# Kernel optimization log

Measured on AMD Instinct MI355X. Metric: run time of the kernel, lower is better.

Reference implementation:

```python
import jax, jax.numpy as jnp
import numpy as np

BETA = 0.25


def _nearest(flat, cb):
    # flat: [N, D], cb: [K, D]
    dist = (jnp.sum(flat * flat, axis=1, keepdims=True)
            + jnp.sum(cb * cb, axis=1)
            - 2.0 * flat @ cb.T)  # [N, K]
    inds = jnp.argmin(dist, axis=1)  # [N]
    q = cb[inds]                     # gather == one_hot @ cb
    return q, inds


def _mse(a, b):
    d = a - b
    return jnp.mean(d * d)


def _closeness(latents, q_det, q_noisy=None):
    adj = q_det if q_noisy is None else q_noisy
    return (BETA * _mse(latents, jax.lax.stop_gradient(q_det))
            + _mse(adj, jax.lax.stop_gradient(latents)))


def setup_inputs() -> dict:
    key = jax.random.key(0)
    k1, k2, k3 = jax.random.split(key, 3)
    B, S, C, K, D = 8192, 64, 16, 8192, 1024
    x = jax.random.normal(k1, (B, S, C), dtype=jnp.float32)
    # codebooks initialized uniform(-1/K, 1/K) and mean-centered, as in initial_codebook
    inv = 1.0 / K
    in_cb = jax.random.uniform(k2, (K, D), dtype=jnp.float32, minval=-inv, maxval=inv)
    in_cb = in_cb - jnp.mean(in_cb, axis=0)
    out_cb = jax.random.uniform(k3, (K, D), dtype=jnp.float32, minval=-inv, maxval=inv)
    out_cb = out_cb - jnp.mean(out_cb, axis=0)
    return {"x": x, "in_codebook": in_cb, "out_codebook": out_cb}


def reference(x, in_codebook, out_codebook):
    B, S, C = x.shape
    flat = x.reshape(B, S * C)  # 'b s c -> b (s c)'
    # in-codebook quantization (noisy=False)
    x_q, x_inds = _nearest(flat, in_codebook)
    # reconstruct(encoding_inds): codebook gather (abstract in base class)
    recon = in_codebook[x_inds]
    # out-codebook quantization; noise_std = 0.0 so noisy inds == det inds
    rq_det, r_inds = _nearest(recon, out_codebook)
    rq_noisy = rq_det
    # straight-through output
    out = flat + jax.lax.stop_gradient(rq_noisy - flat)
    loss = (_closeness(flat, rq_det, rq_noisy)
            + _closeness(flat, x_q)
            + _closeness(recon, rq_det, rq_noisy))
    return out.reshape(B, S, C), loss
```

## Files before the change

### kernel.cpp

```cpp
#include <hip/hip_runtime.h>
#include <hip/hip_bf16.h>
#include <stdint.h>

#define N_ROWS 8192
#define DDIM   1024
#define KCB    8192

#define SX   (6.0f / 127.0f)
#define SCB  (1.3e-4f / 127.0f)
#define NS1  (1.0f / (SX  * SCB))
#define NS2  (1.0f / (SCB * SCB))

typedef int   int32x4 __attribute__((ext_vector_type(4)));

__device__ __forceinline__ int quant_pack4(float4 v, float inv) {
  int q0 = (int)rintf(fminf(fmaxf(v.x * inv, -127.f), 127.f));
  int q1 = (int)rintf(fminf(fmaxf(v.y * inv, -127.f), 127.f));
  int q2 = (int)rintf(fminf(fmaxf(v.z * inv, -127.f), 127.f));
  int q3 = (int)rintf(fminf(fmaxf(v.w * inv, -127.f), 127.f));
  return (q0 & 255) | ((q1 & 255) << 8) | ((q2 & 255) << 16) | (q3 << 24);
}

__global__ __launch_bounds__(256) void prep_all(const float* __restrict__ x,
                                                const float* __restrict__ incb,
                                                const float* __restrict__ outcb,
                                                int* __restrict__ x8,
                                                int* __restrict__ incb8,
                                                int* __restrict__ outcb8,
                                                float* __restrict__ norms_in,
                                                float* __restrict__ norms_out) {
  int b = blockIdx.x;
  int t = threadIdx.x;
  if (b >= 2 * KCB) {
    int i = (b - 2 * KCB) * 256 + t;
    float4 v = ((const float4*)x)[i];
    x8[i] = quant_pack4(v, 1.0f / SX);
    return;
  }
  const float* cb = (b < KCB) ? incb : outcb;
  int*  cb8       = (b < KCB) ? incb8 : outcb8;
  float* norms    = (b < KCB) ? norms_in : norms_out;
  float  nscale   = (b < KCB) ? NS1 : NS2;
  int r = (b < KCB) ? b : b - KCB;
  float4 v = ((const float4*)(cb + (size_t)r * DDIM))[t];
  cb8[(size_t)r * 256 + t] = quant_pack4(v, 1.0f / SCB);
  float s = v.x*v.x + v.y*v.y + v.z*v.z + v.w*v.w;
  #pragma unroll
  for (int sh = 32; sh > 0; sh >>= 1) s += __shfl_down(s, sh, 64);
  __shared__ float wsum[4];
  int lane = t & 63, w = t >> 6;
  if (lane == 0) wsum[w] = s;
  __syncthreads();
  if (t == 0) norms[r] = (wsum[0] + wsum[1] + wsum[2] + wsum[3]) * nscale;
}

#define BM 256
#define BN 128
#define BKB 64
#define NT  (DDIM / BKB)

#define AS1 __attribute__((address_space(1)))
#define AS3 __attribute__((address_space(3)))

#define BAR() do { asm volatile("" ::: "memory"); __builtin_amdgcn_s_barrier(); \
                   asm volatile("" ::: "memory"); } while (0)

__global__ __launch_bounds__(512) void gemm_argmin(
    const char* __restrict__ A0, const char* __restrict__ B0,
    const float* __restrict__ n0, unsigned long long* __restrict__ pk0,
    const char* __restrict__ A1, const char* __restrict__ B1,
    const float* __restrict__ n1, unsigned long long* __restrict__ pk1)
{
  __shared__ char As[3][BM * BKB];
  __shared__ char Bs[3][BN * BKB];

  const char* __restrict__ A     = blockIdx.z ? A1 : A0;
  const char* __restrict__ B     = blockIdx.z ? B1 : B0;
  const float* __restrict__ norms = blockIdx.z ? n1 : n0;
  unsigned long long* __restrict__ packed = blockIdx.z ? pk1 : pk0;

  const int t    = threadIdx.x;
  const int lane = t & 63;
  const int wid  = t >> 6;
  const int wr   = wid >> 1, wc = wid & 1;
  const int la   = lane & 15, lg = lane >> 4;
  const int brow = blockIdx.x * BM;
  const int bcol = blockIdx.y * BN;

  const int srow = t >> 2;
  const int scol = (((t & 3) ^ ((srow >> 1) & 3)) << 4);

  #define STAGE(tt, dA, dB) do {                                              \
    const char* ga0 = A + (size_t)(brow + srow)       * DDIM + (tt) * BKB + scol; \
    const char* ga1 = A + (size_t)(brow + 128 + srow) * DDIM + (tt) * BKB + scol; \
    const char* gb  = B + (size_t)(bcol + srow)       * DDIM + (tt) * BKB + scol; \
    __builtin_amdgcn_global_load_lds((AS1 void*)ga0, (AS3 void*)((dA) + t * 16),          16, 0, 0); \
    __builtin_amdgcn_global_load_lds((AS1 void*)ga1, (AS3 void*)((dA) + (512 + t) * 16),  16, 0, 0); \
    __builtin_amdgcn_global_load_lds((AS1 void*)gb,  (AS3 void*)((dB) + t * 16),          16, 0, 0); \
  } while (0)

  int aoff[4], boff[4];
  #pragma unroll
  for (int mi = 0; mi < 4; ++mi) {
    int r = wr * 64 + mi * 16 + la;
    aoff[mi] = r * BKB + ((lg ^ ((r >> 1) & 3)) << 4);
  }
  #pragma unroll
  for (int ni = 0; ni < 4; ++ni) {
    int r = wc * 64 + ni * 16 + la;
    boff[ni] = r * BKB + ((lg ^ ((r >> 1) & 3)) << 4);
  }

  int32x4 acc[4][4];
  #pragma unroll
  for (int i = 0; i < 4; ++i)
    #pragma unroll
    for (int j = 0; j < 4; ++j) acc[i][j] = (int32x4){0, 0, 0, 0};

  STAGE(0, As[0], Bs[0]);
  STAGE(1, As[1], Bs[1]);
  asm volatile("s_waitcnt vmcnt(3)" ::: "memory");
  BAR();

  for (int kt = 0; kt < NT; ++kt) {
    int nx = kt + 2;
    if (nx < NT) {
      int bi = nx % 3;
      STAGE(nx, As[bi], Bs[bi]);
    }
    const char* curA = As[kt % 3];
    const char* curB = Bs[kt % 3];
    int32x4 af[4], bfr[4];
    #pragma unroll
    for (int mi = 0; mi < 4; ++mi) af[mi]  = *(const int32x4*)(curA + aoff[mi]);
    #pragma unroll
    for (int ni = 0; ni < 4; ++ni) bfr[ni] = *(const int32x4*)(curB + boff[ni]);
    #pragma unroll
    for (int mi = 0; mi < 4; ++mi)
      #pragma unroll
      for (int ni = 0; ni < 4; ++ni)
        acc[mi][ni] = __builtin_amdgcn_mfma_i32_16x16x64_i8(af[mi], bfr[ni], acc[mi][ni], 0, 0, 0);
    if (kt < NT - 2)       { asm volatile("s_waitcnt vmcnt(3)" ::: "memory"); BAR(); }
    else if (kt == NT - 2) { asm volatile("s_waitcnt vmcnt(0)" ::: "memory"); BAR(); }
  }
  #undef STAGE

  float nrm[4]; int colg[4];
  #pragma unroll
  for (int ni = 0; ni < 4; ++ni) {
    colg[ni] = bcol + wc * 64 + ni * 16 + la;
    nrm[ni]  = norms[colg[ni]];
  }
  #pragma unroll
  for (int mi = 0; mi < 4; ++mi) {
    #pragma unroll
    for (int j = 0; j < 4; ++j) {
      float best = nrm[0] - 2.0f * (float)acc[mi][0][j];
      int  bidx  = colg[0];
      #pragma unroll
      for (int ni = 1; ni < 4; ++ni) {
        float v = nrm[ni] - 2.0f * (float)acc[mi][ni][j];
        if (v < best || (v == best && colg[ni] < bidx)) { best = v; bidx = colg[ni]; }
      }
      #pragma unroll
      for (int s = 1; s < 16; s <<= 1) {
        float ov = __shfl_xor(best, s, 64);
        int   oi = __shfl_xor(bidx, s, 64);
        if (ov < best || (ov == best && oi < bidx)) { best = ov; bidx = oi; }
      }
      if (la == 0) {
        int row = brow + wr * 64 + mi * 16 + lg * 4 + j;
        unsigned int ub = __float_as_uint(best);
        ub = (ub & 0x80000000u) ? ~ub : (ub | 0x80000000u);
        unsigned long long pk = ((unsigned long long)ub << 32) | (unsigned int)bidx;
        atomicMin(packed + row, pk);
      }
    }
  }
}

__global__ __launch_bounds__(256) void finalize_k(const float* __restrict__ x,
                                                  const float* __restrict__ incb,
                                                  const float* __restrict__ outcb,
                                                  const unsigned long long* __restrict__ p1,
                                                  const unsigned long long* __restrict__ p2,
                                                  float* __restrict__ out,
                                                  double* __restrict__ accum) {
  int n  = blockIdx.x;
  int xi = (int)(p1[n] & 0xffffffffull);
  int ri = (int)(p2[xi] & 0xffffffffull);
  int t  = threadIdx.x;
  float4 f = ((const float4*)(x     + (size_t)n  * DDIM))[t];
  float4 a = ((const float4*)(incb  + (size_t)xi * DDIM))[t];
  float4 r = ((const float4*)(outcb + (size_t)ri * DDIM))[t];
  ((float4*)(out + (size_t)n * DDIM))[t] = r;
  float s = 0.f;
  { float d1 = f.x - r.x, d2 = f.x - a.x, d3 = a.x - r.x; s += d1*d1 + d2*d2 + d3*d3; }
  { float d1 = f.y - r.y, d2 = f.y - a.y, d3 = a.y - r.y; s += d1*d1 + d2*d2 + d3*d3; }
  { float d1 = f.z - r.z, d2 = f.z - a.z, d3 = a.z - r.z; s += d1*d1 + d2*d2 + d3*d3; }
  { float d1 = f.w - r.w, d2 = f.w - a.w, d3 = a.w - r.w; s += d1*d1 + d2*d2 + d3*d3; }
  #pragma unroll
  for (int sh = 32; sh > 0; sh >>= 1) s += __shfl_down(s, sh, 64);
  __shared__ float wsum[4];
  int lane = t & 63, w = t >> 6;
  if (lane == 0) wsum[w] = s;
  __syncthreads();
  if (t == 0) atomicAdd(accum, (double)(wsum[0] + wsum[1] + wsum[2] + wsum[3]));
}

__global__ void write_loss(const double* __restrict__ accum, float* __restrict__ loss_out) {
  *loss_out = (float)(1.25 * (*accum) / (double)((size_t)N_ROWS * DDIM));
}

extern "C" void kernel_launch(void* const* d_in, const int* in_sizes, int n_in,
                              void* d_out, int out_size, void* d_ws, size_t ws_size,
                              hipStream_t stream) {
  const float* x     = (const float*)d_in[0];
  const float* incb  = (const float*)d_in[1];
  const float* outcb = (const float*)d_in[2];
  float* out = (float*)d_out;
  char*  ws  = (char*)d_ws;
  const size_t MB = 1024 * 1024;

  char* flat8  = ws;
  char* incb8  = ws + 8  * MB;
  char* outcb8 = ws + 16 * MB;
  float* norms_in  = (float*)(ws + 24 * MB);
  float* norms_out = norms_in + KCB;
  unsigned long long* p1 = (unsigned long long*)(ws + 24 * MB + 64 * 1024);
  unsigned long long* p2 = p1 + N_ROWS;
  double* accum = (double*)(p2 + KCB);

  hipMemsetAsync(p1, 0xFF, (N_ROWS + KCB) * sizeof(unsigned long long), stream);
  hipMemsetAsync(accum, 0, sizeof(double), stream);

  prep_all<<<2 * KCB + N_ROWS * DDIM / 1024, 256, 0, stream>>>(
      x, incb, outcb, (int*)flat8, (int*)incb8, (int*)outcb8, norms_in, norms_out);

  gemm_argmin<<<dim3(N_ROWS / BM, KCB / BN, 2), 512, 0, stream>>>(
      flat8, incb8, norms_in,  p1,
      incb8, outcb8, norms_out, p2);

  finalize_k<<<N_ROWS, 256, 0, stream>>>(x, incb, outcb, p1, p2, out, accum);
  write_loss<<<1, 1, 0, stream>>>(accum, out + (size_t)N_ROWS * DDIM);
}
```

Baseline: 324.3 us.

## Switch int8 GEMM to 32x32x32 MFMA and fold init/loss launches into kernels

Replaces the 16x16x64 int8 MFMA tiles with 32x32x32 int8 MFMA, using 2x2 accumulators per wave with an adjusted LDS swizzle and a rewritten argmin epilogue. The two memsets move into prep_all, and the separate write_loss kernel is replaced by a last-block ticket in finalize_k. The aim is fewer LDS fragment loads per MFMA and fewer launches, at the cost of a more involved epilogue row mapping. The tie-break inside the first per-lane compare now drops the index check, though colg[0] < colg[1] always holds there.

```diff
diff --git a/kernel.cpp b/kernel.cpp
--- a/kernel.cpp
+++ b/kernel.cpp
@@ -11,7 +11,8 @@
 #define NS1  (1.0f / (SX  * SCB))
 #define NS2  (1.0f / (SCB * SCB))
 
-typedef int   int32x4 __attribute__((ext_vector_type(4)));
+typedef int int32x4  __attribute__((ext_vector_type(4)));
+typedef int int32x16 __attribute__((ext_vector_type(16)));
 
 __device__ __forceinline__ int quant_pack4(float4 v, float inv) {
   int q0 = (int)rintf(fminf(fmaxf(v.x * inv, -127.f), 127.f));
@@ -28,9 +29,14 @@
                                                 int* __restrict__ incb8,
                                                 int* __restrict__ outcb8,
                                                 float* __restrict__ norms_in,
-                                                float* __restrict__ norms_out) {
+                                                float* __restrict__ norms_out,
+                                                unsigned long long* __restrict__ pinit,
+                                                double* __restrict__ accum,
+                                                unsigned* __restrict__ ticket) {
   int b = blockIdx.x;
   int t = threadIdx.x;
+  if (b == 0 && t == 2) { *accum = 0.0; *ticket = 0u; }
+  if (b < 2 * KCB && t == 1) pinit[b] = ~0ull;
   if (b >= 2 * KCB) {
     int i = (b - 2 * KCB) * 256 + t;
     float4 v = ((const float4*)x)[i];
@@ -58,6 +64,7 @@
 #define BN 128
 #define BKB 64
 #define NT  (DDIM / BKB)
+#define SWZ2(r) ((((r) >> 1) ^ ((r) >> 3)) & 3)
 
 #define AS1 __attribute__((address_space(1)))
 #define AS3 __attribute__((address_space(3)))
@@ -83,12 +90,13 @@
   const int lane = t & 63;
   const int wid  = t >> 6;
   const int wr   = wid >> 1, wc = wid & 1;
-  const int la   = lane & 15, lg = lane >> 4;
+  const int l31  = lane & 31;
+  const int half = lane >> 5;
   const int brow = blockIdx.x * BM;
   const int bcol = blockIdx.y * BN;
 
   const int srow = t >> 2;
-  const int scol = (((t & 3) ^ ((srow >> 1) & 3)) << 4);
+  const int scol = (((t & 3) ^ SWZ2(srow)) << 4);
 
   #define STAGE(tt, dA, dB) do {                                              \
     const char* ga0 = A + (size_t)(brow + srow)       * DDIM + (tt) * BKB + scol; \
@@ -99,23 +107,25 @@
     __builtin_amdgcn_global_load_lds((AS1 void*)gb,  (AS3 void*)((dB) + t * 16),          16, 0, 0); \
   } while (0)
 
-  int aoff[4], boff[4];
-  #pragma unroll
-  for (int mi = 0; mi < 4; ++mi) {
-    int r = wr * 64 + mi * 16 + la;
-    aoff[mi] = r * BKB + ((lg ^ ((r >> 1) & 3)) << 4);
-  }
-  #pragma unroll
-  for (int ni = 0; ni < 4; ++ni) {
-    int r = wc * 64 + ni * 16 + la;
-    boff[ni] = r * BKB + ((lg ^ ((r >> 1) & 3)) << 4);
-  }
-
-  int32x4 acc[4][4];
-  #pragma unroll
-  for (int i = 0; i < 4; ++i)
+  int aoff[2], boff[2];
+  #pragma unroll
+  for (int mi = 0; mi < 2; ++mi) {
+    int r = wr * 64 + mi * 32 + l31;
+    aoff[mi] = r * BKB + ((half ^ SWZ2(r)) << 4);
+  }
+  #pragma unroll
+  for (int ni = 0; ni < 2; ++ni) {
+    int r = wc * 64 + ni * 32 + l31;
+    boff[ni] = r * BKB + ((half ^ SWZ2(r)) << 4);
+  }
+
+  int32x16 acc[2][2];
+  #pragma unroll
+  for (int i = 0; i < 2; ++i)
     #pragma unroll
-    for (int j = 0; j < 4; ++j) acc[i][j] = (int32x4){0, 0, 0, 0};
+    for (int j = 0; j < 2; ++j)
+      #pragma unroll
+      for (int q = 0; q < 16; ++q) acc[i][j][q] = 0;
 
   STAGE(0, As[0], Bs[0]);
   STAGE(1, As[1], Bs[1]);
@@ -130,46 +140,46 @@
     }
     const char* curA = As[kt % 3];
     const char* curB = Bs[kt % 3];
-    int32x4 af[4], bfr[4];
     #pragma unroll
-    for (int mi = 0; mi < 4; ++mi) af[mi]  = *(const int32x4*)(curA + aoff[mi]);
-    #pragma unroll
-    for (int ni = 0; ni < 4; ++ni) bfr[ni] = *(const int32x4*)(curB + boff[ni]);
-    #pragma unroll
-    for (int mi = 0; mi < 4; ++mi)
-      #pragma unroll
-      for (int ni = 0; ni < 4; ++ni)
-        acc[mi][ni] = __builtin_amdgcn_mfma_i32_16x16x64_i8(af[mi], bfr[ni], acc[mi][ni], 0, 0, 0);
+    for (int ks = 0; ks < 2; ++ks) {
+      int32x4 af[2], bfr[2];
+      #pragma unroll
+      for (int mi = 0; mi < 2; ++mi) af[mi]  = *(const int32x4*)(curA + (aoff[mi] ^ (ks << 5)));
+      #pragma unroll
+      for (int ni = 0; ni < 2; ++ni) bfr[ni] = *(const int32x4*)(curB + (boff[ni] ^ (ks << 5)));
+      #pragma unroll
+      for (int mi = 0; mi < 2; ++mi)
+        #pragma unroll
+        for (int ni = 0; ni < 2; ++ni)
+          acc[mi][ni] = __builtin_amdgcn_mfma_i32_32x32x32_i8(af[mi], bfr[ni], acc[mi][ni], 0, 0, 0);
+    }
     if (kt < NT - 2)       { asm volatile("s_waitcnt vmcnt(3)" ::: "memory"); BAR(); }
     else if (kt == NT - 2) { asm volatile("s_waitcnt vmcnt(0)" ::: "memory"); BAR(); }
   }
   #undef STAGE
 
-  float nrm[4]; int colg[4];
-  #pragma unroll
-  for (int ni = 0; ni < 4; ++ni) {
-    colg[ni] = bcol + wc * 64 + ni * 16 + la;
+  float nrm[2]; int colg[2];
+  #pragma unroll
+  for (int ni = 0; ni < 2; ++ni) {
+    colg[ni] = bcol + wc * 64 + ni * 32 + l31;
     nrm[ni]  = norms[colg[ni]];
   }
   #pragma unroll
-  for (int mi = 0; mi < 4; ++mi) {
+  for (int mi = 0; mi < 2; ++mi) {
     #pragma unroll
-    for (int j = 0; j < 4; ++j) {
-      float best = nrm[0] - 2.0f * (float)acc[mi][0][j];
-      int  bidx  = colg[0];
-      #pragma unroll
-      for (int ni = 1; ni < 4; ++ni) {
-        float v = nrm[ni] - 2.0f * (float)acc[mi][ni][j];
-        if (v < best || (v == best && colg[ni] < bidx)) { best = v; bidx = colg[ni]; }
-      }
-      #pragma unroll
-      for (int s = 1; s < 16; s <<= 1) {
+    for (int j = 0; j < 16; ++j) {
+      float v0 = nrm[0] - 2.0f * (float)acc[mi][0][j];
+      float v1 = nrm[1] - 2.0f * (float)acc[mi][1][j];
+      float best = v0; int bidx = colg[0];
+      if (v1 < v0) { best = v1; bidx = colg[1]; }
+      #pragma unroll
+      for (int s = 1; s < 32; s <<= 1) {
         float ov = __shfl_xor(best, s, 64);
         int   oi = __shfl_xor(bidx, s, 64);
         if (ov < best || (ov == best && oi < bidx)) { best = ov; bidx = oi; }
       }
-      if (la == 0) {
-        int row = brow + wr * 64 + mi * 16 + lg * 4 + j;
+      if (l31 == 0) {
+        int row = brow + wr * 64 + mi * 32 + (j & 3) + 8 * (j >> 2) + 4 * half;
         unsigned int ub = __float_as_uint(best);
         ub = (ub & 0x80000000u) ? ~ub : (ub | 0x80000000u);
         unsigned long long pk = ((unsigned long long)ub << 32) | (unsigned int)bidx;
@@ -185,7 +195,8 @@
                                                   const unsigned long long* __restrict__ p1,
                                                   const unsigned long long* __restrict__ p2,
                                                   float* __restrict__ out,
-                                                  double* __restrict__ accum) {
+                                                  double* __restrict__ accum,
+                                                  unsigned* __restrict__ ticket) {
   int n  = blockIdx.x;
   int xi = (int)(p1[n] & 0xffffffffull);
   int ri = (int)(p2[xi] & 0xffffffffull);
@@ -205,11 +216,16 @@
   int lane = t & 63, w = t >> 6;
   if (lane == 0) wsum[w] = s;
   __syncthreads();
-  if (t == 0) atomicAdd(accum, (double)(wsum[0] + wsum[1] + wsum[2] + wsum[3]));
-}
-
-__global__ void write_loss(const double* __restrict__ accum, float* __restrict__ loss_out) {
-  *loss_out = (float)(1.25 * (*accum) / (double)((size_t)N_ROWS * DDIM));
+  if (t == 0) {
+    atomicAdd(accum, (double)(wsum[0] + wsum[1] + wsum[2] + wsum[3]));
+    __threadfence();
+    unsigned old = atomicAdd(ticket, 1u);
+    if (old == gridDim.x - 1) {
+      __threadfence();
+      double tot = atomicAdd(accum, 0.0);
+      out[(size_t)N_ROWS * DDIM] = (float)(1.25 * tot / (double)((size_t)N_ROWS * DDIM));
+    }
+  }
 }
 
 extern "C" void kernel_launch(void* const* d_in, const int* in_sizes, int n_in,
@@ -229,18 +245,16 @@
   float* norms_out = norms_in + KCB;
   unsigned long long* p1 = (unsigned long long*)(ws + 24 * MB + 64 * 1024);
   unsigned long long* p2 = p1 + N_ROWS;
-  double* accum = (double*)(p2 + KCB);
-
-  hipMemsetAsync(p1, 0xFF, (N_ROWS + KCB) * sizeof(unsigned long long), stream);
-  hipMemsetAsync(accum, 0, sizeof(double), stream);
+  double*   accum  = (double*)(p2 + KCB);
+  unsigned* ticket = (unsigned*)(accum + 1);
 
   prep_all<<<2 * KCB + N_ROWS * DDIM / 1024, 256, 0, stream>>>(
-      x, incb, outcb, (int*)flat8, (int*)incb8, (int*)outcb8, norms_in, norms_out);
+      x, incb, outcb, (int*)flat8, (int*)incb8, (int*)outcb8,
+      norms_in, norms_out, p1, accum, ticket);
 
   gemm_argmin<<<dim3(N_ROWS / BM, KCB / BN, 2), 512, 0, stream>>>(
       flat8, incb8, norms_in,  p1,
       incb8, outcb8, norms_out, p2);
 
-  finalize_k<<<N_ROWS, 256, 0, stream>>>(x, incb, outcb, p1, p2, out, accum);
-  write_loss<<<1, 1, 0, stream>>>(accum, out + (size_t)N_ROWS * DDIM);
-}
+  finalize_k<<<N_ROWS, 256, 0, stream>>>(x, incb, outcb, p1, p2, out, accum, ticket);
+}
```

New measurement: 581.1 us. +79.2%, slower.
